# Optimization experiments

Measured on AMD Instinct MI355X. Metric: run time of the kernel, lower is better.

Reference implementation:

```python
import jax, jax.numpy as jnp
import numpy as np

N = 500_000      # num nodes
E = 8_000_000    # num edges (before self-loops)
F_IN, H, C = 16, 8, 2


def setup_inputs() -> dict:
    key = jax.random.key(0)
    k = jax.random.split(key, 6)
    x = jax.random.normal(k[0], (N, F_IN), dtype=jnp.float32)
    edge_index = jax.random.randint(k[1], (2, E), 0, N, dtype=jnp.int32)
    # Glorot-style init like PyG GCNConv
    W1 = jax.random.normal(k[2], (F_IN, H), dtype=jnp.float32) * (1.0 / np.sqrt(F_IN))
    b1 = jnp.zeros((H,), dtype=jnp.float32)
    W2 = jax.random.normal(k[3], (H, C), dtype=jnp.float32) * (1.0 / np.sqrt(H))
    b2 = jnp.zeros((C,), dtype=jnp.float32)
    return {"x": x, "W1": W1, "b1": b1, "W2": W2, "b2": b2, "edge_index": edge_index}


def reference(x, W1, b1, W2, b2, edge_index):
    # GCNConv: out = D^{-1/2} (A + I) D^{-1/2} X W + b   (PyG semantics)
    row, col = edge_index[0], edge_index[1]           # messages flow row -> col
    loop = jnp.arange(N, dtype=row.dtype)
    row = jnp.concatenate([row, loop])                # add self-loops
    col = jnp.concatenate([col, loop])
    deg = jax.ops.segment_sum(jnp.ones_like(col, dtype=x.dtype), col, num_segments=N)
    dinv = jnp.where(deg > 0, jax.lax.rsqrt(deg), jnp.zeros_like(deg))
    norm = dinv[row] * dinv[col]                      # [E+N]

    def propagate(h):  # h: [N, d] -> normalized scatter-add aggregation
        msg = h[row] * norm[:, None]                  # gather + scale, [E+N, d]
        return jax.ops.segment_sum(msg, col, num_segments=N)

    h = jax.nn.relu(propagate(x @ W1) + b1)           # [N, 8]
    out = propagate(h @ W2) + b2                      # [N, 2]
    return jax.nn.log_softmax(out, axis=1)
```

## Files before the change

### kernel.cpp

```cpp
#include <hip/hip_runtime.h>

#define TPB 256
#define NBLK_EDGE 1024
#define CHUNKE 8192
#define BIN_SHIFT 9
#define BIN_SIZE 512
#define MAXK 1024
#define ROW_BITS 19
#define ROW_MASK ((1u << ROW_BITS) - 1)
#define Q_SHIFT 17
#define NKEY 2048
#define CAP 12288

typedef _Float16 half8  __attribute__((ext_vector_type(8)));
typedef _Float16 half2v __attribute__((ext_vector_type(2)));

__global__ void k_zero_int(int* __restrict__ p, int n) {
    int i = blockIdx.x * blockDim.x + threadIdx.x;
    if (i < n) p[i] = 0;
}

__global__ void k_hist(const int* __restrict__ col, int E, int chunk, int K,
                       int* __restrict__ cntB, int* __restrict__ cntT) {
    __shared__ int lh[MAXK];
    int blk = blockIdx.x;
    for (int k = threadIdx.x; k < MAXK; k += blockDim.x) lh[k] = 0;
    __syncthreads();
    int s = blk * chunk, e_ = min(s + chunk, E);
    for (int e = s + threadIdx.x; e < e_; e += blockDim.x)
        atomicAdd(&lh[col[e] >> BIN_SHIFT], 1);
    __syncthreads();
    for (int k = threadIdx.x; k < MAXK; k += blockDim.x) {
        int v = lh[k];
        cntB[(size_t)blk * MAXK + k] = v;
        cntT[(size_t)k * NBLK_EDGE + blk] = v;
    }
}

__global__ void k_colscan(int* __restrict__ cntT, int* __restrict__ ghist) {
    __shared__ int part[256];
    int b = blockIdx.x, tid = threadIdx.x;
    size_t base = (size_t)b * NBLK_EDGE;
    int t4 = tid * 4;
    int c0 = cntT[base + t4], c1 = cntT[base + t4 + 1],
        c2 = cntT[base + t4 + 2], c3 = cntT[base + t4 + 3];
    int sum = c0 + c1 + c2 + c3;
    part[tid] = sum;
    __syncthreads();
    for (int off = 1; off < 256; off <<= 1) {
        int v = (tid >= off) ? part[tid - off] : 0;
        __syncthreads();
        part[tid] += v;
        __syncthreads();
    }
    int excl = part[tid] - sum;
    cntT[base + t4]     = excl;
    cntT[base + t4 + 1] = excl + c0;
    cntT[base + t4 + 2] = excl + c0 + c1;
    cntT[base + t4 + 3] = excl + c0 + c1 + c2;
    if (tid == 255) ghist[b] = part[255];
}

__global__ void k_scan(const int* __restrict__ ghist, int K, int* __restrict__ binBase) {
    __shared__ int tmp[MAXK];
    int tid = threadIdx.x;
    int val = (tid < K) ? ghist[tid] : 0;
    tmp[tid] = val;
    __syncthreads();
    for (int off = 1; off < MAXK; off <<= 1) {
        int v = (tid >= off) ? tmp[tid - off] : 0;
        __syncthreads();
        tmp[tid] += v;
        __syncthreads();
    }
    int incl = tmp[tid];
    if (tid < K) binBase[tid] = incl - val;
    if (tid == K - 1) binBase[K] = incl;
}

__global__ void __launch_bounds__(512) k_reorder(
        const int* __restrict__ row, const int* __restrict__ col,
        int E, int chunk, int K,
        const int* __restrict__ binBase, const int* __restrict__ cntB,
        const int* __restrict__ cntT, unsigned* __restrict__ packed) {
    __shared__ unsigned sorted[CHUNKE];
    __shared__ unsigned short sbin[CHUNKE];
    __shared__ int lcur[MAXK], lbase[MAXK], gbase[MAXK];
    __shared__ int part[512];
    int blk = blockIdx.x, tid = threadIdx.x;
    int s = blk * chunk, e_ = min(s + chunk, E), len = e_ - s;
    int t2 = tid * 2;
    size_t bb = (size_t)blk * MAXK;
    int c0 = cntB[bb + t2], c1 = cntB[bb + t2 + 1];
    int sum = c0 + c1;
    part[tid] = sum;
    __syncthreads();
    for (int off = 1; off < 512; off <<= 1) {
        int v = (tid >= off) ? part[tid - off] : 0;
        __syncthreads();
        part[tid] += v;
        __syncthreads();
    }
    int run = part[tid] - sum;
    lbase[t2] = run;          lcur[t2] = run;
    lbase[t2 + 1] = run + c0; lcur[t2 + 1] = run + c0;
    for (int k = tid; k < K; k += blockDim.x)
        gbase[k] = binBase[k] + cntT[(size_t)k * NBLK_EDGE + blk];
    __syncthreads();
    for (int i = tid; i < len; i += blockDim.x) {
        int cc = col[s + i];
        int b = cc >> BIN_SHIFT;
        int slot = atomicAdd(&lcur[b], 1);
        sorted[slot] = ((unsigned)(cc & (BIN_SIZE - 1)) << ROW_BITS) | (unsigned)row[s + i];
        sbin[slot] = (unsigned short)b;
    }
    __syncthreads();
    for (int i = tid; i < len; i += blockDim.x) {
        int b = sbin[i];
        packed[gbase[b] + (i - lbase[b])] = sorted[i];
    }
}

__global__ void __launch_bounds__(1024) k_binsort_deg(
        unsigned* __restrict__ packed, const int* __restrict__ binBase,
        unsigned* __restrict__ scratch, int* __restrict__ scratchCur,
        float* __restrict__ dinv, int* __restrict__ keyptr, int N, int E, int K) {
    __shared__ unsigned buf2[CAP];
    __shared__ int cnt[NKEY], cur[NKEY];
    __shared__ int part[1024];
    __shared__ int sbShared;
    int tid = threadIdx.x;
    int bin = blockIdx.x;
    int s = binBase[bin], t = binBase[bin + 1];
    int len = t - s;
    bool fast = (len <= CAP);
    cnt[tid] = 0;
    cnt[tid + 1024] = 0;
    if (!fast && tid == 0) sbShared = atomicAdd(scratchCur, len);
    __syncthreads();
    for (int i = tid; i < len; i += blockDim.x) {
        unsigned v = packed[s + i];
        int k = (int)((v >> ROW_BITS) << 2) | (int)((v & ROW_MASK) >> Q_SHIFT);
        atomicAdd(&cnt[k], 1);
    }
    __syncthreads();
    int t2 = tid * 2;
    int c0 = cnt[t2], c1 = cnt[t2 + 1];
    int sum = c0 + c1;
    part[tid] = sum;
    __syncthreads();
    for (int off = 1; off < 1024; off <<= 1) {
        int v = (tid >= off) ? part[tid - off] : 0;
        __syncthreads();
        part[tid] += v;
        __syncthreads();
    }
    int excl = part[tid] - sum;
    cur[t2] = excl;
    cur[t2 + 1] = excl + c0;
    int base = bin << BIN_SHIFT;
    if (base + (t2 >> 2) < N) keyptr[((size_t)bin << 11) + t2] = s + excl;
    if (base + ((t2 + 1) >> 2) < N) keyptr[((size_t)bin << 11) + t2 + 1] = s + excl + c0;
    if (tid < BIN_SIZE) {
        int node = base + tid;
        if (node < N) {
            int deg = cnt[4 * tid] + cnt[4 * tid + 1] + cnt[4 * tid + 2] + cnt[4 * tid + 3];
            dinv[node] = rsqrtf((float)(deg + 1));
        }
    }
    if (bin == K - 1 && tid == 0) keyptr[(size_t)4 * N] = E;
    __syncthreads();
    if (fast) {
        for (int i = tid; i < len; i += blockDim.x) {
            unsigned v = packed[s + i];
            int k = (int)((v >> ROW_BITS) << 2) | (int)((v & ROW_MASK) >> Q_SHIFT);
            int slot = atomicAdd(&cur[k], 1);
            buf2[slot] = v;
        }
        __syncthreads();
        for (int i = tid; i < len; i += blockDim.x) packed[s + i] = buf2[i];
    } else {
        unsigned* stg = scratch + sbShared;
        for (int i = tid; i < len; i += blockDim.x) stg[i] = packed[s + i];
        __threadfence();
        __syncthreads();
        for (int i = tid; i < len; i += blockDim.x) {
            unsigned v = stg[i];
            int k = (int)((v >> ROW_BITS) << 2) | (int)((v & ROW_MASK) >> Q_SHIFT);
            int slot = atomicAdd(&cur[k], 1);
            packed[s + slot] = v;
        }
    }
}

__global__ void k_node1(const float* __restrict__ x, const float* __restrict__ W1,
                        const float* __restrict__ dinv_arr, half8* __restrict__ g0, int N) {
    int i = blockIdx.x * blockDim.x + threadIdx.x;
    if (i >= N) return;
    float di = dinv_arr[i];
    const float4* xv = (const float4*)(x + (size_t)i * 16);
    float4 a0 = xv[0], a1 = xv[1], a2 = xv[2], a3 = xv[3];
    float xl[16] = {a0.x, a0.y, a0.z, a0.w, a1.x, a1.y, a1.z, a1.w,
                    a2.x, a2.y, a2.z, a2.w, a3.x, a3.y, a3.z, a3.w};
    float h[8];
#pragma unroll
    for (int j = 0; j < 8; ++j) h[j] = 0.0f;
#pragma unroll
    for (int k = 0; k < 16; ++k) {
        float xk = xl[k];
#pragma unroll
        for (int j = 0; j < 8; ++j) h[j] += xk * W1[k * 8 + j];
    }
    half8 g;
#pragma unroll
    for (int j = 0; j < 8; ++j) g[j] = (_Float16)(di * h[j]);
    g0[i] = g;
}

__global__ void k_gather1_phase(const unsigned* __restrict__ packed,
                                const int* __restrict__ keyptr,
                                const half8* __restrict__ g0,
                                const float* __restrict__ dinv_arr,
                                const float* __restrict__ b1,
                                const float* __restrict__ W2,
                                float* __restrict__ accA,
                                half2v* __restrict__ g1, int N, int q) {
    int i = blockIdx.x * blockDim.x + threadIdx.x;
    if (i >= N) return;
    int s = keyptr[4 * i + q], t = keyptr[4 * i + q + 1];
    float acc[8];
    if (q == 0) {
#pragma unroll
        for (int j = 0; j < 8; ++j) acc[j] = 0.0f;
    } else {
        const float4* av = (const float4*)(accA + (size_t)i * 8);
        float4 lo = av[0], hi = av[1];
        acc[0] = lo.x; acc[1] = lo.y; acc[2] = lo.z; acc[3] = lo.w;
        acc[4] = hi.x; acc[5] = hi.y; acc[6] = hi.z; acc[7] = hi.w;
    }
    int e = s;
    for (; e + 4 <= t; e += 4) {
        unsigned p0 = packed[e], p1 = packed[e + 1], p2 = packed[e + 2], p3 = packed[e + 3];
        half8 v0 = g0[p0 & ROW_MASK];
        half8 v1 = g0[p1 & ROW_MASK];
        half8 v2 = g0[p2 & ROW_MASK];
        half8 v3 = g0[p3 & ROW_MASK];
#pragma unroll
        for (int j = 0; j < 8; ++j)
            acc[j] += (float)v0[j] + (float)v1[j] + (float)v2[j] + (float)v3[j];
    }
    for (; e < t; ++e) {
        half8 v = g0[packed[e] & ROW_MASK];
#pragma unroll
        for (int j = 0; j < 8; ++j) acc[j] += (float)v[j];
    }
    if (q < 3) {
        float4* av = (float4*)(accA + (size_t)i * 8);
        av[0] = make_float4(acc[0], acc[1], acc[2], acc[3]);
        av[1] = make_float4(acc[4], acc[5], acc[6], acc[7]);
    } else {
        half8 self = g0[i];
        float di = dinv_arr[i];
        float o0 = 0.0f, o1 = 0.0f;
#pragma unroll
        for (int j = 0; j < 8; ++j) {
            float hj = fmaxf(di * (acc[j] + (float)self[j]) + b1[j], 0.0f);
            o0 += hj * W2[j * 2 + 0];
            o1 += hj * W2[j * 2 + 1];
        }
        half2v g;
        g.x = (_Float16)(di * o0);
        g.y = (_Float16)(di * o1);
        g1[i] = g;
    }
}

__global__ void k_gather2_final(const unsigned* __restrict__ packed,
                                const int* __restrict__ keyptr,
                                const half2v* __restrict__ g1,
                                const float* __restrict__ dinv_arr,
                                const float* __restrict__ b2,
                                float* __restrict__ out, int N) {
    int i = blockIdx.x * blockDim.x + threadIdx.x;
    if (i >= N) return;
    int s = keyptr[4 * i], t = keyptr[4 * i + 4];
    half2v sg = g1[i];
    float a0 = (float)sg.x, a1 = (float)sg.y;
    int e = s;
    for (; e + 4 <= t; e += 4) {
        unsigned p0 = packed[e], p1 = packed[e + 1], p2 = packed[e + 2], p3 = packed[e + 3];
        half2v v0 = g1[p0 & ROW_MASK];
        half2v v1 = g1[p1 & ROW_MASK];
        half2v v2 = g1[p2 & ROW_MASK];
        half2v v3 = g1[p3 & ROW_MASK];
        a0 += (float)v0.x + (float)v1.x + (float)v2.x + (float)v3.x;
        a1 += (float)v0.y + (float)v1.y + (float)v2.y + (float)v3.y;
    }
    for (; e < t; ++e) {
        half2v v = g1[packed[e] & ROW_MASK];
        a0 += (float)v.x;
        a1 += (float)v.y;
    }
    float di = dinv_arr[i];
    float o0 = di * a0 + b2[0];
    float o1 = di * a1 + b2[1];
    float m = fmaxf(o0, o1);
    float lse = m + logf(expf(o0 - m) + expf(o1 - m));
    ((float2*)out)[i] = make_float2(o0 - lse, o1 - lse);
}

extern "C" void kernel_launch(void* const* d_in, const int* in_sizes, int n_in,
                              void* d_out, int out_size, void* d_ws, size_t ws_size,
                              hipStream_t stream) {
    const float* x  = (const float*)d_in[0];
    const float* W1 = (const float*)d_in[1];
    const float* b1 = (const float*)d_in[2];
    const float* W2 = (const float*)d_in[3];
    const float* b2 = (const float*)d_in[4];
    const int*   ei = (const int*)d_in[5];

    const int N = in_sizes[0] / 16;
    const int E = in_sizes[5] / 2;
    const int* row = ei;
    const int* col = ei + E;
    const int K = (N + BIN_SIZE - 1) >> BIN_SHIFT;

    float* ws   = (float*)d_ws;
    float* dinv = ws;
    half8* g0   = (half8*)(ws + (size_t)N);
    half2v* g1  = (half2v*)(ws + (size_t)5 * N);
    float* accA = ws + (size_t)6 * N;
    int* keyptr = (int*)(ws + (size_t)14 * N);
    int*   meta = (int*)(ws + (size_t)18 * N + 8);
    int* ghist      = meta;
    int* binBase    = meta + MAXK;
    int* scratchCur = meta + 2 * MAXK + 16;
    unsigned* packed = (unsigned*)(meta + 3 * MAXK);
    int* cntB = (int*)(packed + E);
    int* cntT = cntB + (size_t)MAXK * NBLK_EDGE;

    float* out = (float*)d_out;

    const int gN = (N + TPB - 1) / TPB;
    const int chunk = (E + NBLK_EDGE - 1) / NBLK_EDGE;

    k_zero_int   <<<1, 64, 0, stream>>>(scratchCur, 1);
    k_hist       <<<NBLK_EDGE, TPB, 0, stream>>>(col, E, chunk, K, cntB, cntT);
    k_colscan    <<<K, 256, 0, stream>>>(cntT, ghist);
    k_scan       <<<1, MAXK, 0, stream>>>(ghist, K, binBase);
    k_reorder    <<<NBLK_EDGE, 512, 0, stream>>>(row, col, E, chunk, K,
                                                 binBase, cntB, cntT, packed);
    k_binsort_deg<<<K, 1024, 0, stream>>>(packed, binBase, (unsigned*)g0, scratchCur,
                                          dinv, keyptr, N, E, K);
    k_node1      <<<gN, TPB, 0, stream>>>(x, W1, dinv, g0, N);
    for (int q = 0; q < 4; ++q)
        k_gather1_phase<<<gN, TPB, 0, stream>>>(packed, keyptr, g0, dinv, b1, W2,
                                                accA, g1, N, q);
    k_gather2_final<<<gN, TPB, 0, stream>>>(packed, keyptr, g1, dinv, b2, out, N);
}
```

Baseline: 379.6 us.

## Fuse node transform into binsort, fold zeroing into scan, widen reorder blocks

The separate node-transform kernel (x·W1 scaled by dinv, stored as fp16) now runs at the tail of the per-bin sort kernel, so dinv is used straight from registers. The overflow scratch buffer moves from g0 to accA so g0 can be written in the same kernel. The scratch-counter reset moves into the scan kernel, removing a tiny launch. The reorder kernel goes to 1024 threads, one bin per thread for its local scan, to cut scan steps. Together these remove two launches and one dinv round trip, at the cost of extra register pressure in the 1024-thread binsort kernel.

Result: faster. 371.1 us (-2.2%).

```diff
diff --git a/kernel.cpp b/kernel.cpp
--- a/kernel.cpp
+++ b/kernel.cpp
@@ -15,11 +15,6 @@
 typedef _Float16 half8  __attribute__((ext_vector_type(8)));
 typedef _Float16 half2v __attribute__((ext_vector_type(2)));
 
-__global__ void k_zero_int(int* __restrict__ p, int n) {
-    int i = blockIdx.x * blockDim.x + threadIdx.x;
-    if (i < n) p[i] = 0;
-}
-
 __global__ void k_hist(const int* __restrict__ col, int E, int chunk, int K,
                        int* __restrict__ cntB, int* __restrict__ cntT) {
     __shared__ int lh[MAXK];
@@ -61,9 +56,11 @@
     if (tid == 255) ghist[b] = part[255];
 }
 
-__global__ void k_scan(const int* __restrict__ ghist, int K, int* __restrict__ binBase) {
+__global__ void k_scan(const int* __restrict__ ghist, int K, int* __restrict__ binBase,
+                       int* __restrict__ scratchCur) {
     __shared__ int tmp[MAXK];
     int tid = threadIdx.x;
+    if (tid == 0) *scratchCur = 0;
     int val = (tid < K) ? ghist[tid] : 0;
     tmp[tid] = val;
     __syncthreads();
@@ -78,7 +75,7 @@
     if (tid == K - 1) binBase[K] = incl;
 }
 
-__global__ void __launch_bounds__(512) k_reorder(
+__global__ void __launch_bounds__(1024) k_reorder(
         const int* __restrict__ row, const int* __restrict__ col,
         int E, int chunk, int K,
         const int* __restrict__ binBase, const int* __restrict__ cntB,
@@ -86,26 +83,23 @@
     __shared__ unsigned sorted[CHUNKE];
     __shared__ unsigned short sbin[CHUNKE];
     __shared__ int lcur[MAXK], lbase[MAXK], gbase[MAXK];
-    __shared__ int part[512];
+    __shared__ int part[1024];
     int blk = blockIdx.x, tid = threadIdx.x;
     int s = blk * chunk, e_ = min(s + chunk, E), len = e_ - s;
-    int t2 = tid * 2;
     size_t bb = (size_t)blk * MAXK;
-    int c0 = cntB[bb + t2], c1 = cntB[bb + t2 + 1];
-    int sum = c0 + c1;
-    part[tid] = sum;
-    __syncthreads();
-    for (int off = 1; off < 512; off <<= 1) {
+    int c0 = cntB[bb + tid];
+    part[tid] = c0;
+    __syncthreads();
+    for (int off = 1; off < 1024; off <<= 1) {
         int v = (tid >= off) ? part[tid - off] : 0;
         __syncthreads();
         part[tid] += v;
         __syncthreads();
     }
-    int run = part[tid] - sum;
-    lbase[t2] = run;          lcur[t2] = run;
-    lbase[t2 + 1] = run + c0; lcur[t2 + 1] = run + c0;
-    for (int k = tid; k < K; k += blockDim.x)
-        gbase[k] = binBase[k] + cntT[(size_t)k * NBLK_EDGE + blk];
+    int excl = part[tid] - c0;
+    lbase[tid] = excl;
+    lcur[tid] = excl;
+    gbase[tid] = binBase[tid] + cntT[(size_t)tid * NBLK_EDGE + blk];
     __syncthreads();
     for (int i = tid; i < len; i += blockDim.x) {
         int cc = col[s + i];
@@ -124,7 +118,9 @@
 __global__ void __launch_bounds__(1024) k_binsort_deg(
         unsigned* __restrict__ packed, const int* __restrict__ binBase,
         unsigned* __restrict__ scratch, int* __restrict__ scratchCur,
-        float* __restrict__ dinv, int* __restrict__ keyptr, int N, int E, int K) {
+        const float* __restrict__ x, const float* __restrict__ W1,
+        float* __restrict__ dinv, half8* __restrict__ g0,
+        int* __restrict__ keyptr, int N, int E, int K) {
     __shared__ unsigned buf2[CAP];
     __shared__ int cnt[NKEY], cur[NKEY];
     __shared__ int part[1024];
@@ -161,12 +157,12 @@
     int base = bin << BIN_SHIFT;
     if (base + (t2 >> 2) < N) keyptr[((size_t)bin << 11) + t2] = s + excl;
     if (base + ((t2 + 1) >> 2) < N) keyptr[((size_t)bin << 11) + t2 + 1] = s + excl + c0;
-    if (tid < BIN_SIZE) {
-        int node = base + tid;
-        if (node < N) {
-            int deg = cnt[4 * tid] + cnt[4 * tid + 1] + cnt[4 * tid + 2] + cnt[4 * tid + 3];
-            dinv[node] = rsqrtf((float)(deg + 1));
-        }
+    float di = 0.0f;
+    int node = base + tid;
+    if (tid < BIN_SIZE && node < N) {
+        int deg = cnt[4 * tid] + cnt[4 * tid + 1] + cnt[4 * tid + 2] + cnt[4 * tid + 3];
+        di = rsqrtf((float)(deg + 1));
+        dinv[node] = di;
     }
     if (bin == K - 1 && tid == 0) keyptr[(size_t)4 * N] = E;
     __syncthreads();
@@ -191,30 +187,25 @@
             packed[s + slot] = v;
         }
     }
-}
-
-__global__ void k_node1(const float* __restrict__ x, const float* __restrict__ W1,
-                        const float* __restrict__ dinv_arr, half8* __restrict__ g0, int N) {
-    int i = blockIdx.x * blockDim.x + threadIdx.x;
-    if (i >= N) return;
-    float di = dinv_arr[i];
-    const float4* xv = (const float4*)(x + (size_t)i * 16);
-    float4 a0 = xv[0], a1 = xv[1], a2 = xv[2], a3 = xv[3];
-    float xl[16] = {a0.x, a0.y, a0.z, a0.w, a1.x, a1.y, a1.z, a1.w,
-                    a2.x, a2.y, a2.z, a2.w, a3.x, a3.y, a3.z, a3.w};
-    float h[8];
-#pragma unroll
-    for (int j = 0; j < 8; ++j) h[j] = 0.0f;
-#pragma unroll
-    for (int k = 0; k < 16; ++k) {
-        float xk = xl[k];
-#pragma unroll
-        for (int j = 0; j < 8; ++j) h[j] += xk * W1[k * 8 + j];
-    }
-    half8 g;
-#pragma unroll
-    for (int j = 0; j < 8; ++j) g[j] = (_Float16)(di * h[j]);
-    g0[i] = g;
+    if (tid < BIN_SIZE && node < N) {
+        const float4* xv = (const float4*)(x + (size_t)node * 16);
+        float h[8];
+#pragma unroll
+        for (int j = 0; j < 8; ++j) h[j] = 0.0f;
+#pragma unroll
+        for (int kk = 0; kk < 4; ++kk) {
+            float4 a = xv[kk];
+            int kb = kk * 4;
+#pragma unroll
+            for (int j = 0; j < 8; ++j)
+                h[j] += a.x * W1[kb * 8 + j] + a.y * W1[(kb + 1) * 8 + j]
+                      + a.z * W1[(kb + 2) * 8 + j] + a.w * W1[(kb + 3) * 8 + j];
+        }
+        half8 g;
+#pragma unroll
+        for (int j = 0; j < 8; ++j) g[j] = (_Float16)(di * h[j]);
+        g0[node] = g;
+    }
 }
 
 __global__ void k_gather1_phase(const unsigned* __restrict__ packed,
@@ -344,15 +335,13 @@
     const int gN = (N + TPB - 1) / TPB;
     const int chunk = (E + NBLK_EDGE - 1) / NBLK_EDGE;
 
-    k_zero_int   <<<1, 64, 0, stream>>>(scratchCur, 1);
     k_hist       <<<NBLK_EDGE, TPB, 0, stream>>>(col, E, chunk, K, cntB, cntT);
     k_colscan    <<<K, 256, 0, stream>>>(cntT, ghist);
-    k_scan       <<<1, MAXK, 0, stream>>>(ghist, K, binBase);
-    k_reorder    <<<NBLK_EDGE, 512, 0, stream>>>(row, col, E, chunk, K,
-                                                 binBase, cntB, cntT, packed);
-    k_binsort_deg<<<K, 1024, 0, stream>>>(packed, binBase, (unsigned*)g0, scratchCur,
-                                          dinv, keyptr, N, E, K);
-    k_node1      <<<gN, TPB, 0, stream>>>(x, W1, dinv, g0, N);
+    k_scan       <<<1, MAXK, 0, stream>>>(ghist, K, binBase, scratchCur);
+    k_reorder    <<<NBLK_EDGE, 1024, 0, stream>>>(row, col, E, chunk, K,
+                                                  binBase, cntB, cntT, packed);
+    k_binsort_deg<<<K, 1024, 0, stream>>>(packed, binBase, (unsigned*)accA, scratchCur,
+                                          x, W1, dinv, g0, keyptr, N, E, K);
     for (int q = 0; q < 4; ++q)
         k_gather1_phase<<<gN, TPB, 0, stream>>>(packed, keyptr, g0, dinv, b1, W2,
                                                 accA, g1, N, q);
```
